# Kernel optimization log

Hardware: AMD Instinct MI355X
Metric: run time of the kernel (lower is better)

## Reference

```python
import jax, jax.numpy as jnp
import numpy as np
import math

HEADS = 8
EMBED = 512
HEAD_DIM = EMBED // HEADS
N, L = 2, 256


def setup_inputs() -> dict:
    key = jax.random.key(0)
    ks = jax.random.split(key, 16)
    s = 0.05  # weight scale for numerical stability
    inp = {
        "values": jax.random.normal(ks[0], (N, L, EMBED), jnp.float32),
        "keys": jax.random.normal(ks[1], (N, L, EMBED), jnp.float32),
        "query": jax.random.normal(ks[2], (N, L, EMBED), jnp.float32),
        "pos": jax.random.normal(ks[3], (N, L, EMBED), jnp.float32),
        "rel": jax.random.normal(ks[4], (N, L, L, EMBED), jnp.float32),
        "mask": jnp.ones((N, L), jnp.float32),
        "Wv": jax.random.normal(ks[5], (HEAD_DIM, HEAD_DIM), jnp.float32) * s,
        "Wk": jax.random.normal(ks[6], (HEAD_DIM, HEAD_DIM), jnp.float32) * s,
        "Wq": jax.random.normal(ks[7], (HEAD_DIM, HEAD_DIM), jnp.float32) * s,
        "Wpq": jax.random.normal(ks[8], (HEAD_DIM, HEAD_DIM), jnp.float32) * s,
        "Wpk": jax.random.normal(ks[9], (HEAD_DIM, HEAD_DIM), jnp.float32) * s,
        "Wrk": jax.random.normal(ks[10], (HEAD_DIM, HEAD_DIM), jnp.float32) * s,
        "Wrq": jax.random.normal(ks[11], (HEAD_DIM, HEAD_DIM), jnp.float32) * s,
        "Wout": jax.random.normal(ks[12], (EMBED, EMBED), jnp.float32) * s,
        "bout": jnp.zeros((EMBED,), jnp.float32),
    }
    return inp


def reference(values, keys, query, pos, rel, mask, Wv, Wk, Wq, Wpq, Wpk, Wrk, Wrq, Wout, bout):
    n, lq, e = query.shape
    h, d = HEADS, e // HEADS
    # split heads; per-head Linear shares one [d,d] weight (y = x @ W.T)
    v = values.reshape(n, -1, h, d) @ Wv.T
    k = keys.reshape(n, -1, h, d) @ Wk.T
    q = query.reshape(n, lq, h, d) @ Wq.T
    p = pos.reshape(n, lq, h, d)
    r = rel.reshape(n, lq, lq, h, d)
    # mode == 'all': QK + pos-pos + two relative terms
    scores = jnp.einsum('nqhd,nkhd->nhqk', q, k)
    pq = p @ Wpq.T
    pk = p @ Wpk.T
    pos_scores = jnp.einsum('nqhd,nkhd->nhqk', pq, pk)
    rk = r @ Wrk.T
    rq = r @ Wrq.T
    rel1 = jnp.einsum('nqhd,nqkhd->nhqk', q, rk)
    rel2 = jnp.einsum('nqkhd,nkhd->nhqk', rq, k)
    energy = (scores + pos_scores + rel1 + rel2) / math.sqrt(2.0)
    energy = energy + (1.0 - mask)[:, None, None, :] * (-1e9)
    attn = jax.nn.softmax(energy, axis=3)
    out = jnp.einsum('nhqk,nkhd->nqhd', attn, v).reshape(n, lq, e)
    return out @ Wout.T + bout
```

## Files before the change

### kernel.cpp

```cpp
#include <hip/hip_runtime.h>
#include <hip/hip_bf16.h>

#define NB 2
#define L 256
#define H 8
#define D 64
#define E 512
#define NL (NB * L)
#define RSQRT2 0.70710678118654752f

__global__ __launch_bounds__(256) void k0_transpose(const float* __restrict__ Wout,
                                                    float* __restrict__ WoutT) {
    __shared__ float tile[64][65];
    int t = threadIdx.x;
    int bi = blockIdx.x >> 3;
    int bj = blockIdx.x & 7;
    int tx = t & 63, ty = t >> 6;
#pragma unroll
    for (int m = 0; m < 16; m++) {
        int el = ty + (m << 2);
        tile[el][tx] = Wout[(size_t)(bi * 64 + el) * E + bj * 64 + tx];
    }
    __syncthreads();
#pragma unroll
    for (int m = 0; m < 16; m++) {
        int cl = ty + (m << 2);
        WoutT[(size_t)(bj * 64 + cl) * E + bi * 64 + tx] = tile[tx][cl];
    }
}

__device__ __forceinline__ float dot64(const float* __restrict__ a,
                                       const float* __restrict__ w) {
    const float4* a4 = (const float4*)a;
    const float4* w4 = (const float4*)w;
    float acc = 0.f;
#pragma unroll
    for (int j = 0; j < 16; j++) {
        float4 x = a4[j], y = w4[j];
        acc = fmaf(x.x, y.x, acc);
        acc = fmaf(x.y, y.y, acc);
        acc = fmaf(x.z, y.z, acc);
        acc = fmaf(x.w, y.w, acc);
    }
    return acc;
}

__global__ __launch_bounds__(256) void k1_proj(
    const float* __restrict__ values, const float* __restrict__ keys,
    const float* __restrict__ query, const float* __restrict__ pos,
    const float* __restrict__ Wv, const float* __restrict__ Wk,
    const float* __restrict__ Wq, const float* __restrict__ Wpq,
    const float* __restrict__ Wpk, const float* __restrict__ Wrk,
    const float* __restrict__ Wrq,
    float* __restrict__ qv_ws, float* __restrict__ kv_ws,
    float* __restrict__ vv_ws, float* __restrict__ pq_ws,
    float* __restrict__ pk_ws, float* __restrict__ qrk_ws,
    float* __restrict__ krq_ws) {
    __shared__ float xq[E], xk[E], xv[E], xp[E];
    __shared__ float qs[E], ks[E];
    int t = threadIdx.x;
    int nl = blockIdx.x;
    size_t base = (size_t)nl * E;
    for (int j = t; j < E; j += 256) {
        xq[j] = query[base + j];
        xk[j] = keys[base + j];
        xv[j] = values[base + j];
        xp[j] = pos[base + j];
    }
    __syncthreads();
#pragma unroll
    for (int cc = 0; cc < 2; cc++) {
        int c = t + cc * 256;
        int h = c >> 6, i = c & 63;
        const float* xqh = xq + (h << 6);
        const float* xkh = xk + (h << 6);
        const float* xvh = xv + (h << 6);
        const float* xph = xp + (h << 6);
        float q_c = dot64(xqh, Wq + (i << 6));
        float k_c = dot64(xkh, Wk + (i << 6));
        float v_c = dot64(xvh, Wv + (i << 6));
        float pq_c = dot64(xph, Wpq + (i << 6));
        float pk_c = dot64(xph, Wpk + (i << 6));
        qv_ws[base + c] = q_c;
        kv_ws[base + c] = k_c;
        vv_ws[base + c] = v_c;
        pq_ws[base + c] = pq_c;
        pk_ws[base + c] = pk_c;
        qs[c] = q_c;
        ks[c] = k_c;
    }
    __syncthreads();
#pragma unroll
    for (int cc = 0; cc < 2; cc++) {
        int c = t + cc * 256;
        int h = c >> 6, d = c & 63;
        float aq = 0.f, ak = 0.f;
        const float* qh = qs + (h << 6);
        const float* kh = ks + (h << 6);
#pragma unroll 8
        for (int i = 0; i < 64; i++) {
            aq = fmaf(qh[i], Wrk[(i << 6) + d], aq);
            ak = fmaf(kh[i], Wrq[(i << 6) + d], ak);
        }
        qrk_ws[base + c] = aq;
        krq_ws[base + c] = ak;
    }
}

__global__ __launch_bounds__(256) void k2a_energy(
    const float* __restrict__ rel, const float* __restrict__ mask,
    const float* __restrict__ qv_ws, const float* __restrict__ kv_ws,
    const float* __restrict__ pq_ws, const float* __restrict__ pk_ws,
    const float* __restrict__ qrk_ws, const float* __restrict__ krq_ws,
    float* __restrict__ e_ws) {
    int t = threadIdx.x;
    int b = blockIdx.x;
    int kc = b & 7;
    int nq = b >> 3;
    int n = nq >> 8;

    int lane128 = t & 127;
    int rowsel = t >> 7;
    int cq = lane128 << 2;
    int h = lane128 >> 4;
    int sub = t & 15;

    float4 qrk4 = *(const float4*)(qrk_ws + (size_t)nq * E + cq);
    float4 qv4 = *(const float4*)(qv_ws + (size_t)nq * E + cq);
    float4 pq4 = *(const float4*)(pq_ws + (size_t)nq * E + cq);

    const float* relb = rel + (size_t)nq * L * E;
    size_t nbase = ((size_t)n << 8);
    float* eb = e_ws + (size_t)nq * (H * L);

#pragma unroll 4
    for (int kk = 0; kk < 16; kk++) {
        int k = (kc << 5) + (kk << 1) + rowsel;
        float4 r4 = *(const float4*)(relb + ((size_t)k << 9) + cq);
        float4 kq4 = *(const float4*)(krq_ws + (nbase + k) * E + cq);
        float4 kp4 = *(const float4*)(kv_ws + (nbase + k) * E + cq);
        float4 pk4 = *(const float4*)(pk_ws + (nbase + k) * E + cq);
        float p;
        p = r4.x * (qrk4.x + kq4.x);
        p = fmaf(r4.y, (qrk4.y + kq4.y), p);
        p = fmaf(r4.z, (qrk4.z + kq4.z), p);
        p = fmaf(r4.w, (qrk4.w + kq4.w), p);
        p = fmaf(kp4.x, qv4.x, p);
        p = fmaf(kp4.y, qv4.y, p);
        p = fmaf(kp4.z, qv4.z, p);
        p = fmaf(kp4.w, qv4.w, p);
        p = fmaf(pk4.x, pq4.x, p);
        p = fmaf(pk4.y, pq4.y, p);
        p = fmaf(pk4.z, pq4.z, p);
        p = fmaf(pk4.w, pq4.w, p);
        p += __shfl_down(p, 8, 16);
        p += __shfl_down(p, 4, 16);
        p += __shfl_down(p, 2, 16);
        p += __shfl_down(p, 1, 16);
        if (sub == 0) {
            eb[(h << 8) + k] = p * RSQRT2 + (1.0f - mask[(n << 8) + k]) * (-1e9f);
        }
    }
}

__global__ __launch_bounds__(512) void k2b_soft_av(
    const float* __restrict__ e_ws, const float* __restrict__ vv_ws,
    float* __restrict__ attn_ws) {
    __shared__ float e_s[H * L];
    __shared__ float inv_s[H];
    int t = threadIdx.x;
    int nq = blockIdx.x;
    int n = nq >> 8;

    ((float4*)e_s)[t] = ((const float4*)(e_ws + (size_t)nq * (H * L)))[t];
    __syncthreads();

    {
        int hh = t >> 6;
        int lane = t & 63;
        float* eh = e_s + (hh << 8);
        float m = -INFINITY;
#pragma unroll
        for (int j = 0; j < 4; j++) m = fmaxf(m, eh[lane + (j << 6)]);
#pragma unroll
        for (int off = 32; off > 0; off >>= 1) m = fmaxf(m, __shfl_xor(m, off, 64));
        float s = 0.f;
#pragma unroll
        for (int j = 0; j < 4; j++) {
            int idx = lane + (j << 6);
            float ev = __expf(eh[idx] - m);
            eh[idx] = ev;
            s += ev;
        }
#pragma unroll
        for (int off = 32; off > 0; off >>= 1) s += __shfl_xor(s, off, 64);
        if (lane == 0) inv_s[hh] = 1.0f / s;
    }
    __syncthreads();

    {
        int c = t;
        int h1 = t >> 6;
        const float* eh = e_s + (h1 << 8);
        float acc = 0.f;
        const float* vb = vv_ws + (((size_t)n << 8) * E);
#pragma unroll 8
        for (int k = 0; k < L; k++) {
            acc = fmaf(eh[k], vb[((size_t)k << 9) + c], acc);
        }
        attn_ws[(size_t)nq * E + c] = acc * inv_s[h1];
    }
}

__global__ __launch_bounds__(512) void k3_out(const float* __restrict__ attn_ws,
                                              const float* __restrict__ WoutT,
                                              const float* __restrict__ bout,
                                              float* __restrict__ out) {
    __shared__ float As[E];
    int t = threadIdx.x;
    int r = blockIdx.x;
    As[t] = attn_ws[(size_t)r * E + t];
    __syncthreads();
    float acc = bout[t];
#pragma unroll 8
    for (int c = 0; c < E; c++) {
        acc = fmaf(As[c], WoutT[((size_t)c << 9) + t], acc);
    }
    out[(size_t)r * E + t] = acc;
}

extern "C" void kernel_launch(void* const* d_in, const int* in_sizes, int n_in,
                              void* d_out, int out_size, void* d_ws, size_t ws_size,
                              hipStream_t stream) {
    const float* values = (const float*)d_in[0];
    const float* keys = (const float*)d_in[1];
    const float* query = (const float*)d_in[2];
    const float* pos = (const float*)d_in[3];
    const float* rel = (const float*)d_in[4];
    const float* mask = (const float*)d_in[5];
    const float* Wv = (const float*)d_in[6];
    const float* Wk = (const float*)d_in[7];
    const float* Wq = (const float*)d_in[8];
    const float* Wpq = (const float*)d_in[9];
    const float* Wpk = (const float*)d_in[10];
    const float* Wrk = (const float*)d_in[11];
    const float* Wrq = (const float*)d_in[12];
    const float* Wout = (const float*)d_in[13];
    const float* bout = (const float*)d_in[14];
    float* out = (float*)d_out;

    float* ws = (float*)d_ws;
    const size_t SZ = (size_t)NL * E;
    float* qv_ws = ws + 0 * SZ;
    float* kv_ws = ws + 1 * SZ;
    float* vv_ws = ws + 2 * SZ;
    float* pq_ws = ws + 3 * SZ;
    float* pk_ws = ws + 4 * SZ;
    float* qrk_ws = ws + 5 * SZ;
    float* krq_ws = ws + 6 * SZ;
    float* attn_ws = ws + 7 * SZ;
    float* WoutT = ws + 8 * SZ;
    float* e_ws = ws + 9 * SZ;

    k0_transpose<<<64, 256, 0, stream>>>(Wout, WoutT);
    k1_proj<<<NL, 256, 0, stream>>>(values, keys, query, pos, Wv, Wk, Wq, Wpq,
                                    Wpk, Wrk, Wrq, qv_ws, kv_ws, vv_ws, pq_ws,
                                    pk_ws, qrk_ws, krq_ws);
    k2a_energy<<<NL * 8, 256, 0, stream>>>(rel, mask, qv_ws, kv_ws, pq_ws,
                                           pk_ws, qrk_ws, krq_ws, e_ws);
    k2b_soft_av<<<NL, 512, 0, stream>>>(e_ws, vv_ws, attn_ws);
    k3_out<<<NL, 512, 0, stream>>>(attn_ws, WoutT, bout, out);
}
```

Before: 517.9 us.

## Tile energy kernel over q and k blocks; batch four rows per output block

The energy kernel now processes a 16x16 tile of query and key positions per block. It keeps the key-side projected vectors and mask terms in registers and reuses them across 16 queries, instead of reloading them for each query. The output projection computes four rows per block so each Wout load is shared by four accumulators. Both changes cut grid sizes sharply, which may reduce memory-level parallelism in the bandwidth-bound rel stream.

```diff
diff --git a/kernel.cpp b/kernel.cpp
--- a/kernel.cpp
+++ b/kernel.cpp
@@ -107,7 +107,7 @@
     }
 }
 
-__global__ __launch_bounds__(256) void k2a_energy(
+__global__ __launch_bounds__(256, 2) void k2a_energy(
     const float* __restrict__ rel, const float* __restrict__ mask,
     const float* __restrict__ qv_ws, const float* __restrict__ kv_ws,
     const float* __restrict__ pq_ws, const float* __restrict__ pk_ws,
@@ -115,50 +115,66 @@
     float* __restrict__ e_ws) {
     int t = threadIdx.x;
     int b = blockIdx.x;
-    int kc = b & 7;
-    int nq = b >> 3;
-    int n = nq >> 8;
+    int kc = b & 15;
+    int qt = (b >> 4) & 15;
+    int n = b >> 8;
 
     int lane128 = t & 127;
     int rowsel = t >> 7;
     int cq = lane128 << 2;
     int h = lane128 >> 4;
     int sub = t & 15;
-
-    float4 qrk4 = *(const float4*)(qrk_ws + (size_t)nq * E + cq);
-    float4 qv4 = *(const float4*)(qv_ws + (size_t)nq * E + cq);
-    float4 pq4 = *(const float4*)(pq_ws + (size_t)nq * E + cq);
-
-    const float* relb = rel + (size_t)nq * L * E;
-    size_t nbase = ((size_t)n << 8);
-    float* eb = e_ws + (size_t)nq * (H * L);
-
-#pragma unroll 4
-    for (int kk = 0; kk < 16; kk++) {
-        int k = (kc << 5) + (kk << 1) + rowsel;
-        float4 r4 = *(const float4*)(relb + ((size_t)k << 9) + cq);
-        float4 kq4 = *(const float4*)(krq_ws + (nbase + k) * E + cq);
-        float4 kp4 = *(const float4*)(kv_ws + (nbase + k) * E + cq);
-        float4 pk4 = *(const float4*)(pk_ws + (nbase + k) * E + cq);
-        float p;
-        p = r4.x * (qrk4.x + kq4.x);
-        p = fmaf(r4.y, (qrk4.y + kq4.y), p);
-        p = fmaf(r4.z, (qrk4.z + kq4.z), p);
-        p = fmaf(r4.w, (qrk4.w + kq4.w), p);
-        p = fmaf(kp4.x, qv4.x, p);
-        p = fmaf(kp4.y, qv4.y, p);
-        p = fmaf(kp4.z, qv4.z, p);
-        p = fmaf(kp4.w, qv4.w, p);
-        p = fmaf(pk4.x, pq4.x, p);
-        p = fmaf(pk4.y, pq4.y, p);
-        p = fmaf(pk4.z, pq4.z, p);
-        p = fmaf(pk4.w, pq4.w, p);
-        p += __shfl_down(p, 8, 16);
-        p += __shfl_down(p, 4, 16);
-        p += __shfl_down(p, 2, 16);
-        p += __shfl_down(p, 1, 16);
-        if (sub == 0) {
-            eb[(h << 8) + k] = p * RSQRT2 + (1.0f - mask[(n << 8) + k]) * (-1e9f);
+    size_t nbase = (size_t)n << 8;
+    int kb = kc << 4;
+
+    float4 kq[8], kp[8], pk[8];
+    float mk[8];
+#pragma unroll
+    for (int jj = 0; jj < 8; jj++) {
+        int k = kb + (jj << 1) + rowsel;
+        kq[jj] = *(const float4*)(krq_ws + (nbase + k) * E + cq);
+        kp[jj] = *(const float4*)(kv_ws + (nbase + k) * E + cq);
+        pk[jj] = *(const float4*)(pk_ws + (nbase + k) * E + cq);
+        mk[jj] = (1.0f - mask[nbase + k]) * (-1e9f);
+    }
+
+    for (int qi = 0; qi < 16; qi++) {
+        int q = (qt << 4) + qi;
+        size_t nq = nbase + q;
+        float4 qrk4 = *(const float4*)(qrk_ws + nq * E + cq);
+        float4 qv4 = *(const float4*)(qv_ws + nq * E + cq);
+        float4 pq4 = *(const float4*)(pq_ws + nq * E + cq);
+        const float* relb = rel + nq * (size_t)(L * E);
+        float4 r[8];
+#pragma unroll
+        for (int jj = 0; jj < 8; jj++) {
+            int k = kb + (jj << 1) + rowsel;
+            r[jj] = *(const float4*)(relb + ((size_t)k << 9) + cq);
+        }
+        float* eb = e_ws + nq * (H * L);
+#pragma unroll
+        for (int jj = 0; jj < 8; jj++) {
+            float p;
+            p = r[jj].x * (qrk4.x + kq[jj].x);
+            p = fmaf(r[jj].y, (qrk4.y + kq[jj].y), p);
+            p = fmaf(r[jj].z, (qrk4.z + kq[jj].z), p);
+            p = fmaf(r[jj].w, (qrk4.w + kq[jj].w), p);
+            p = fmaf(kp[jj].x, qv4.x, p);
+            p = fmaf(kp[jj].y, qv4.y, p);
+            p = fmaf(kp[jj].z, qv4.z, p);
+            p = fmaf(kp[jj].w, qv4.w, p);
+            p = fmaf(pk[jj].x, pq4.x, p);
+            p = fmaf(pk[jj].y, pq4.y, p);
+            p = fmaf(pk[jj].z, pq4.z, p);
+            p = fmaf(pk[jj].w, pq4.w, p);
+            p += __shfl_down(p, 8, 16);
+            p += __shfl_down(p, 4, 16);
+            p += __shfl_down(p, 2, 16);
+            p += __shfl_down(p, 1, 16);
+            if (sub == 0) {
+                int k = kb + (jj << 1) + rowsel;
+                eb[(h << 8) + k] = p * RSQRT2 + mk[jj];
+            }
         }
     }
 }
@@ -216,17 +232,25 @@
                                               const float* __restrict__ WoutT,
                                               const float* __restrict__ bout,
                                               float* __restrict__ out) {
-    __shared__ float As[E];
-    int t = threadIdx.x;
-    int r = blockIdx.x;
-    As[t] = attn_ws[(size_t)r * E + t];
-    __syncthreads();
-    float acc = bout[t];
+    __shared__ float As[4 * E];
+    int t = threadIdx.x;
+    int r0 = blockIdx.x << 2;
+    for (int j = t; j < 4 * E; j += 512) As[j] = attn_ws[(size_t)r0 * E + j];
+    __syncthreads();
+    float b0 = bout[t];
+    float a0 = b0, a1 = b0, a2 = b0, a3 = b0;
 #pragma unroll 8
     for (int c = 0; c < E; c++) {
-        acc = fmaf(As[c], WoutT[((size_t)c << 9) + t], acc);
-    }
-    out[(size_t)r * E + t] = acc;
+        float w = WoutT[((size_t)c << 9) + t];
+        a0 = fmaf(As[c], w, a0);
+        a1 = fmaf(As[E + c], w, a1);
+        a2 = fmaf(As[2 * E + c], w, a2);
+        a3 = fmaf(As[3 * E + c], w, a3);
+    }
+    out[(size_t)(r0 + 0) * E + t] = a0;
+    out[(size_t)(r0 + 1) * E + t] = a1;
+    out[(size_t)(r0 + 2) * E + t] = a2;
+    out[(size_t)(r0 + 3) * E + t] = a3;
 }
 
 extern "C" void kernel_launch(void* const* d_in, const int* in_sizes, int n_in,
@@ -266,8 +290,8 @@
     k1_proj<<<NL, 256, 0, stream>>>(values, keys, query, pos, Wv, Wk, Wq, Wpq,
                                     Wpk, Wrk, Wrq, qv_ws, kv_ws, vv_ws, pq_ws,
                                     pk_ws, qrk_ws, krq_ws);
-    k2a_energy<<<NL * 8, 256, 0, stream>>>(rel, mask, qv_ws, kv_ws, pq_ws,
-                                           pk_ws, qrk_ws, krq_ws, e_ws);
+    k2a_energy<<<512, 256, 0, stream>>>(rel, mask, qv_ws, kv_ws, pq_ws,
+                                        pk_ws, qrk_ws, krq_ws, e_ws);
     k2b_soft_av<<<NL, 512, 0, stream>>>(e_ws, vv_ws, attn_ws);
-    k3_out<<<NL, 512, 0, stream>>>(attn_ws, WoutT, bout, out);
-}
+    k3_out<<<NL / 4, 512, 0, stream>>>(attn_ws, WoutT, bout, out);
+}
```

New measurement: 491.9 us. 5.0% less time.
